# Kernel optimization log

Hardware: AMD Instinct MI355X
Metric: run time of the kernel (lower is better)

Reference implementation:

```python
import jax, jax.numpy as jnp
import numpy as np

H = 4096   # hidden_size
V = 4      # vocab_size (Dyck-2)
OUT = 4    # output_size
MS = 104   # memory_size (stack depth)
MD = 3     # memory_dim (stack element width)


def setup_inputs() -> dict:
    key = jax.random.key(0)
    ks = jax.random.split(key, 17)
    s = 1.0 / np.sqrt(H)
    f32 = jnp.float32
    return {
        "inp": jax.random.randint(ks[0], (1,), 0, H),
        "hidden0": jax.random.normal(ks[1], (1, 1, H), f32),
        "stack": jax.random.normal(ks[2], (MS, MD), f32),
        "emb": (jax.random.normal(ks[3], (H, V), f32) * s),      # nn.Embedding(H, V)
        "w_ih": (jax.random.normal(ks[4], (3 * H, V), f32) * s),  # GRU input weights
        "w_hh": (jax.random.normal(ks[5], (3 * H, H), f32) * s),  # GRU hidden weights
        "b_ih": (jax.random.normal(ks[6], (3 * H,), f32) * s),
        "b_hh": (jax.random.normal(ks[7], (3 * H,), f32) * s),
        "w_y": (jax.random.normal(ks[8], (OUT, H), f32) * s),
        "b_y": (jax.random.normal(ks[9], (OUT,), f32) * s),
        "w_n": (jax.random.normal(ks[10], (MD, H), f32) * s),
        "b_n": (jax.random.normal(ks[11], (MD,), f32) * s),
        "w_a": (jax.random.normal(ks[12], (2, H), f32) * s),
        "b_a": (jax.random.normal(ks[13], (2,), f32) * s),
        "w_sh": (jax.random.normal(ks[14], (H, MD), f32) * s),
        "b_sh": (jax.random.normal(ks[15], (H,), f32) * s),
    }


def reference(inp, hidden0, stack, emb, w_ih, w_hh, b_ih, b_hh,
              w_y, b_y, w_n, b_n, w_a, b_a, w_sh, b_sh):
    # embedded = embedding(inp).view(1,1,-1) -> work with flat (V,)
    x = emb[inp[0]]                                   # (V,)
    # hidden_bar = W_sh(stack[0]) + hidden0
    h_bar = (w_sh @ stack[0] + b_sh) + hidden0[0, 0]  # (H,)
    # one GRU step (PyTorch gate order: r, z, n)
    gi = w_ih @ x + b_ih                              # (3H,)
    gh = w_hh @ h_bar + b_hh                          # (3H,)
    i_r, i_z, i_n = jnp.split(gi, 3)
    h_r, h_z, h_n = jnp.split(gh, 3)
    r = jax.nn.sigmoid(i_r + h_r)
    z = jax.nn.sigmoid(i_z + h_z)
    n = jnp.tanh(i_n + r * h_n)
    h = (1.0 - z) * n + z * h_bar                     # (H,) = ht = hidden
    # heads
    output = jax.nn.sigmoid(w_y @ h + b_y).reshape(1, OUT)
    action = jax.nn.softmax(w_a @ h + b_a)            # (2,) push/pop weights
    new_elt = jax.nn.sigmoid(w_n @ h + b_n).reshape(1, MD)
    # differentiable stack update
    push_side = jnp.concatenate([new_elt, stack[:-1]], axis=0)          # (MS, MD)
    pop_side = jnp.concatenate([stack[1:], jnp.zeros((1, MD), stack.dtype)], axis=0)
    new_stack = action[0] * push_side + action[1] * pop_side
    hidden = h.reshape(1, 1, H)
    return output, hidden, new_stack
```

## Files before the change

kernel.cpp:

```cpp
#include <hip/hip_runtime.h>
#include <hip/hip_bf16.h>

#define H  4096
#define V  4
#define OUT_N 4
#define MS 104
#define MD 3

__device__ __forceinline__ float b2f(unsigned short u) {
    return __uint_as_float(((unsigned int)u) << 16);
}
__device__ __forceinline__ float ldf(const void* p, size_t i, bool is_f32) {
    return is_f32 ? ((const float*)p)[i] : b2f(((const unsigned short*)p)[i]);
}
__device__ __forceinline__ void stf(void* p, size_t i, bool is_f32, float v) {
    if (is_f32) ((float*)p)[i] = v;
    else        ((__hip_bfloat16*)p)[i] = __float2bfloat16(v);
}

__device__ __forceinline__ bool detect_f32(const void* w_hh) {
    const unsigned short* w = (const unsigned short*)w_hh;
    const int lane = threadIdx.x & 63;
    int bad = 0;
    #pragma unroll
    for (int i = 0; i < 16; ++i) {
        const float v = b2f(w[lane + (i << 6)]);
        if (!(fabsf(v) < 1.0e6f)) bad = 1;
    }
    return __ballot(bad) != 0ull;
}

__device__ __forceinline__ float dot8(uint4 a, float4 h0, float4 h1) {
    return __uint_as_float(a.x << 16)          * h0.x
         + __uint_as_float(a.x & 0xffff0000u)  * h0.y
         + __uint_as_float(a.y << 16)          * h0.z
         + __uint_as_float(a.y & 0xffff0000u)  * h0.w
         + __uint_as_float(a.z << 16)          * h1.x
         + __uint_as_float(a.z & 0xffff0000u)  * h1.y
         + __uint_as_float(a.w << 16)          * h1.z
         + __uint_as_float(a.w & 0xffff0000u)  * h1.w;
}

__global__ __launch_bounds__(256) void hbar_kernel(
    const void* __restrict__ w_sh, const void* __restrict__ b_sh,
    const void* __restrict__ hidden0, const void* __restrict__ stack,
    const void* __restrict__ w_hh, float* __restrict__ h_bar) {
    const bool f32 = detect_f32(w_hh);
    const float s0 = ldf(stack, 0, f32);
    const float s1 = ldf(stack, 1, f32);
    const float s2 = ldf(stack, 2, f32);
    const int j = blockIdx.x * 256 + threadIdx.x;
    h_bar[j] = ldf(w_sh, (size_t)j * 3 + 0, f32) * s0
             + ldf(w_sh, (size_t)j * 3 + 1, f32) * s1
             + ldf(w_sh, (size_t)j * 3 + 2, f32) * s2
             + ldf(b_sh, j, f32) + ldf(hidden0, j, f32);
}

__global__ __launch_bounds__(256) void gru_kernel(
    const int*  __restrict__ inp,  const void* __restrict__ emb,
    const void* __restrict__ w_ih, const void* __restrict__ w_hh,
    const void* __restrict__ b_ih, const void* __restrict__ b_hh,
    const float* __restrict__ h_bar, float* __restrict__ h_f32,
    void* __restrict__ out) {
    const bool f32 = detect_f32(w_hh);
    const int wave = threadIdx.x >> 6, lane = threadIdx.x & 63;
    const int k = (blockIdx.x << 2) + wave;

    float ar = 0.f, az = 0.f, an = 0.f;
    if (f32) {
        const float4* W  = (const float4*)w_hh;
        const float4* HB = (const float4*)h_bar;
        const size_t q0 = (size_t)k           * (H / 4);
        const size_t q1 = (size_t)(k + H)     * (H / 4);
        const size_t q2 = (size_t)(k + 2 * H) * (H / 4);
        #pragma unroll 4
        for (int it = 0; it < H / 256; ++it) {
            const int i = (it << 6) + lane;
            const float4 hb = HB[i];
            const float4 a = W[q0 + i];
            const float4 b = W[q1 + i];
            const float4 c = W[q2 + i];
            ar += a.x * hb.x + a.y * hb.y + a.z * hb.z + a.w * hb.w;
            az += b.x * hb.x + b.y * hb.y + b.z * hb.z + b.w * hb.w;
            an += c.x * hb.x + c.y * hb.y + c.z * hb.z + c.w * hb.w;
        }
    } else {
        const uint4*  W  = (const uint4*)w_hh;
        const float4* HB = (const float4*)h_bar;
        const size_t q0 = (size_t)k           * (H / 8);
        const size_t q1 = (size_t)(k + H)     * (H / 8);
        const size_t q2 = (size_t)(k + 2 * H) * (H / 8);
        #pragma unroll 2
        for (int it = 0; it < H / 512; ++it) {
            const int i = (it << 6) + lane;
            const float4 h0 = HB[2 * i], h1 = HB[2 * i + 1];
            ar += dot8(W[q0 + i], h0, h1);
            az += dot8(W[q1 + i], h0, h1);
            an += dot8(W[q2 + i], h0, h1);
        }
    }

    #pragma unroll
    for (int off = 32; off > 0; off >>= 1) {
        ar += __shfl_down(ar, off);
        az += __shfl_down(az, off);
        an += __shfl_down(an, off);
    }

    if (lane == 0) {
        const int idx = inp[0];
        float x[V];
        #pragma unroll
        for (int c = 0; c < V; ++c) x[c] = ldf(emb, (size_t)idx * V + c, f32);

        float gi[3];
        #pragma unroll
        for (int g = 0; g < 3; ++g) {
            float acc = ldf(b_ih, (size_t)(k + g * H), f32);
            #pragma unroll
            for (int c = 0; c < V; ++c)
                acc += ldf(w_ih, (size_t)(k + g * H) * V + c, f32) * x[c];
            gi[g] = acc;
        }
        const float ghr = ar + ldf(b_hh, (size_t)k,           f32);
        const float ghz = az + ldf(b_hh, (size_t)(k + H),     f32);
        const float ghn = an + ldf(b_hh, (size_t)(k + 2 * H), f32);

        const float r = 1.f / (1.f + expf(-(gi[0] + ghr)));
        const float z = 1.f / (1.f + expf(-(gi[1] + ghz)));
        const float n = tanhf(gi[2] + r * ghn);
        const float hk = (1.f - z) * n + z * h_bar[k];

        h_f32[k] = hk;
        stf(out, (size_t)(OUT_N + k), f32, hk);
    }
}

__global__ __launch_bounds__(1024) void heads_kernel(
    const float* __restrict__ h,
    const void* __restrict__ w_y, const void* __restrict__ b_y,
    const void* __restrict__ w_a, const void* __restrict__ b_a,
    const void* __restrict__ w_n, const void* __restrict__ b_n,
    const void* __restrict__ stack, const void* __restrict__ w_hh,
    void* __restrict__ out) {
    const bool f32 = detect_f32(w_hh);
    const int t = threadIdx.x, wave = t >> 6, lane = t & 63;

    __shared__ float scal[9];
    if (wave < 9) {
        const void* base; size_t row;
        if (wave < 4)      { base = w_y; row = (size_t)wave * H; }
        else if (wave < 6) { base = w_a; row = (size_t)(wave - 4) * H; }
        else               { base = w_n; row = (size_t)(wave - 6) * H; }

        float acc = 0.f;
        if (f32) {
            const float4* W  = (const float4*)((const float*)base + row);
            const float4* Hv = (const float4*)h;
            #pragma unroll 4
            for (int it = 0; it < H / 256; ++it) {
                const int i = (it << 6) + lane;
                const float4 a = W[i], hb = Hv[i];
                acc += a.x * hb.x + a.y * hb.y + a.z * hb.z + a.w * hb.w;
            }
        } else {
            const uint4*  W  = (const uint4*)((const unsigned short*)base + row);
            const float4* Hv = (const float4*)h;
            #pragma unroll 2
            for (int it = 0; it < H / 512; ++it) {
                const int i = (it << 6) + lane;
                acc += dot8(W[i], Hv[2 * i], Hv[2 * i + 1]);
            }
        }
        #pragma unroll
        for (int off = 32; off > 0; off >>= 1) acc += __shfl_down(acc, off);
        if (lane == 0) scal[wave] = acc;
    }
    __syncthreads();

    __shared__ float act0, act1, ne[MD];
    if (t == 0) {
        const float a0 = scal[4] + ldf(b_a, 0, f32);
        const float a1 = scal[5] + ldf(b_a, 1, f32);
        const float m  = fmaxf(a0, a1);
        const float e0 = expf(a0 - m), e1 = expf(a1 - m);
        const float inv = 1.f / (e0 + e1);
        act0 = e0 * inv; act1 = e1 * inv;
    }
    if (t < OUT_N)
        stf(out, (size_t)t, f32,
            1.f / (1.f + expf(-(scal[t] + ldf(b_y, t, f32)))));
    if (t < MD)
        ne[t] = 1.f / (1.f + expf(-(scal[6 + t] + ldf(b_n, t, f32))));
    __syncthreads();

    const float a0 = act0, a1 = act1;
    for (int idx = t; idx < MS * MD; idx += 1024) {
        const int i = idx / MD;
        const int d = idx - i * MD;
        const float push = (i == 0)      ? ne[d] : ldf(stack, (size_t)(idx - MD), f32);
        const float pop  = (i == MS - 1) ? 0.f   : ldf(stack, (size_t)(idx + MD), f32);
        stf(out, (size_t)(OUT_N + H + idx), f32, a0 * push + a1 * pop);
    }
}

extern "C" void kernel_launch(void* const* d_in, const int* in_sizes, int n_in,
                              void* d_out, int out_size, void* d_ws, size_t ws_size,
                              hipStream_t stream) {
    const int* inp      = (const int*)d_in[0];
    const void* hidden0 = d_in[1];
    const void* stack   = d_in[2];
    const void* emb     = d_in[3];
    const void* w_ih    = d_in[4];
    const void* w_hh    = d_in[5];
    const void* b_ih    = d_in[6];
    const void* b_hh    = d_in[7];
    const void* w_y     = d_in[8];
    const void* b_y     = d_in[9];
    const void* w_n     = d_in[10];
    const void* b_n     = d_in[11];
    const void* w_a     = d_in[12];
    const void* b_a     = d_in[13];
    const void* w_sh    = d_in[14];
    const void* b_sh    = d_in[15];

    float* h_bar = (float*)d_ws;
    float* h     = h_bar + H;

    hbar_kernel<<<H / 256, 256, 0, stream>>>(w_sh, b_sh, hidden0, stack,
                                             w_hh, h_bar);
    gru_kernel<<<H / 4, 256, 0, stream>>>(inp, emb, w_ih, w_hh, b_ih, b_hh,
                                          h_bar, h, d_out);
    heads_kernel<<<1, 1024, 0, stream>>>(h, w_y, b_y, w_a, b_a, w_n, b_n,
                                         stack, w_hh, d_out);
}
```

Baseline: 314.1 us.

## Fuse h_bar computation into GRU kernel with LDS-staged hidden vector

Merges the separate h_bar kernel into the GRU matvec kernel. Each block now recomputes the full h_bar vector into shared memory, then assigns one wave per gate row (2 hidden units × 3 gates per block) and reduces through LDS. This removes one launch and the global round trip for h_bar. In exchange, every one of the 2048 blocks redundantly reads w_sh, b_sh and hidden0 before it can start streaming w_hh. The 16KB of LDS per block may also limit occupancy.

```diff
diff --git a/kernel.cpp b/kernel.cpp
--- a/kernel.cpp
+++ b/kernel.cpp
@@ -6,6 +6,9 @@
 #define OUT_N 4
 #define MS 104
 #define MD 3
+
+#define KPB 2
+#define TPB (KPB * 3 * 64)
 
 __device__ __forceinline__ float b2f(unsigned short u) {
     return __uint_as_float(((unsigned int)u) << 16);
@@ -41,73 +44,64 @@
          + __uint_as_float(a.w & 0xffff0000u)  * h1.w;
 }
 
-__global__ __launch_bounds__(256) void hbar_kernel(
+__global__ __launch_bounds__(TPB) void gru_fused_kernel(
+    const int*  __restrict__ inp,  const void* __restrict__ emb,
+    const void* __restrict__ w_ih, const void* __restrict__ w_hh,
+    const void* __restrict__ b_ih, const void* __restrict__ b_hh,
     const void* __restrict__ w_sh, const void* __restrict__ b_sh,
     const void* __restrict__ hidden0, const void* __restrict__ stack,
-    const void* __restrict__ w_hh, float* __restrict__ h_bar) {
+    float* __restrict__ h_f32, void* __restrict__ out) {
     const bool f32 = detect_f32(w_hh);
+    const int t = threadIdx.x;
+    const int wave = t >> 6, lane = t & 63;
+    const int k0 = blockIdx.x * KPB;
+
+    __shared__ float hb_lds[H];
+    __shared__ float red[KPB][3];
+
     const float s0 = ldf(stack, 0, f32);
     const float s1 = ldf(stack, 1, f32);
     const float s2 = ldf(stack, 2, f32);
-    const int j = blockIdx.x * 256 + threadIdx.x;
-    h_bar[j] = ldf(w_sh, (size_t)j * 3 + 0, f32) * s0
-             + ldf(w_sh, (size_t)j * 3 + 1, f32) * s1
-             + ldf(w_sh, (size_t)j * 3 + 2, f32) * s2
-             + ldf(b_sh, j, f32) + ldf(hidden0, j, f32);
-}
-
-__global__ __launch_bounds__(256) void gru_kernel(
-    const int*  __restrict__ inp,  const void* __restrict__ emb,
-    const void* __restrict__ w_ih, const void* __restrict__ w_hh,
-    const void* __restrict__ b_ih, const void* __restrict__ b_hh,
-    const float* __restrict__ h_bar, float* __restrict__ h_f32,
-    void* __restrict__ out) {
-    const bool f32 = detect_f32(w_hh);
-    const int wave = threadIdx.x >> 6, lane = threadIdx.x & 63;
-    const int k = (blockIdx.x << 2) + wave;
-
-    float ar = 0.f, az = 0.f, an = 0.f;
+    for (int j = t; j < H; j += TPB) {
+        hb_lds[j] = ldf(w_sh, (size_t)j * 3 + 0, f32) * s0
+                  + ldf(w_sh, (size_t)j * 3 + 1, f32) * s1
+                  + ldf(w_sh, (size_t)j * 3 + 2, f32) * s2
+                  + ldf(b_sh, j, f32) + ldf(hidden0, j, f32);
+    }
+    __syncthreads();
+
+    const int g  = wave % 3;
+    const int kk = wave / 3;
+    const int row = g * H + k0 + kk;
+
+    float acc = 0.f;
     if (f32) {
-        const float4* W  = (const float4*)w_hh;
-        const float4* HB = (const float4*)h_bar;
-        const size_t q0 = (size_t)k           * (H / 4);
-        const size_t q1 = (size_t)(k + H)     * (H / 4);
-        const size_t q2 = (size_t)(k + 2 * H) * (H / 4);
+        const float4* W  = (const float4*)w_hh + (size_t)row * (H / 4);
+        const float4* HB = (const float4*)hb_lds;
         #pragma unroll 4
         for (int it = 0; it < H / 256; ++it) {
             const int i = (it << 6) + lane;
-            const float4 hb = HB[i];
-            const float4 a = W[q0 + i];
-            const float4 b = W[q1 + i];
-            const float4 c = W[q2 + i];
-            ar += a.x * hb.x + a.y * hb.y + a.z * hb.z + a.w * hb.w;
-            az += b.x * hb.x + b.y * hb.y + b.z * hb.z + b.w * hb.w;
-            an += c.x * hb.x + c.y * hb.y + c.z * hb.z + c.w * hb.w;
+            const float4 a = W[i], hb = HB[i];
+            acc += a.x * hb.x + a.y * hb.y + a.z * hb.z + a.w * hb.w;
         }
     } else {
-        const uint4*  W  = (const uint4*)w_hh;
-        const float4* HB = (const float4*)h_bar;
-        const size_t q0 = (size_t)k           * (H / 8);
-        const size_t q1 = (size_t)(k + H)     * (H / 8);
-        const size_t q2 = (size_t)(k + 2 * H) * (H / 8);
-        #pragma unroll 2
+        const uint4*  W  = (const uint4*)w_hh + (size_t)row * (H / 8);
+        const float4* HB = (const float4*)hb_lds;
+        #pragma unroll 4
         for (int it = 0; it < H / 512; ++it) {
             const int i = (it << 6) + lane;
-            const float4 h0 = HB[2 * i], h1 = HB[2 * i + 1];
-            ar += dot8(W[q0 + i], h0, h1);
-            az += dot8(W[q1 + i], h0, h1);
-            an += dot8(W[q2 + i], h0, h1);
-        }
-    }
-
+            acc += dot8(W[i], HB[2 * i], HB[2 * i + 1]);
+        }
+    }
     #pragma unroll
-    for (int off = 32; off > 0; off >>= 1) {
-        ar += __shfl_down(ar, off);
-        az += __shfl_down(az, off);
-        an += __shfl_down(an, off);
-    }
-
-    if (lane == 0) {
+    for (int off = 32; off > 0; off >>= 1) acc += __shfl_down(acc, off);
+    if (lane == 0) red[kk][g] = acc;
+    __syncthreads();
+
+    if (t < KPB) {
+        const int k = k0 + t;
+        const float sr = red[t][0], sz = red[t][1], sn = red[t][2];
+
         const int idx = inp[0];
         float x[V];
         #pragma unroll
@@ -115,21 +109,21 @@
 
         float gi[3];
         #pragma unroll
-        for (int g = 0; g < 3; ++g) {
-            float acc = ldf(b_ih, (size_t)(k + g * H), f32);
+        for (int gg = 0; gg < 3; ++gg) {
+            float a = ldf(b_ih, (size_t)(k + gg * H), f32);
             #pragma unroll
             for (int c = 0; c < V; ++c)
-                acc += ldf(w_ih, (size_t)(k + g * H) * V + c, f32) * x[c];
-            gi[g] = acc;
-        }
-        const float ghr = ar + ldf(b_hh, (size_t)k,           f32);
-        const float ghz = az + ldf(b_hh, (size_t)(k + H),     f32);
-        const float ghn = an + ldf(b_hh, (size_t)(k + 2 * H), f32);
+                a += ldf(w_ih, (size_t)(k + gg * H) * V + c, f32) * x[c];
+            gi[gg] = a;
+        }
+        const float ghr = sr + ldf(b_hh, (size_t)k,           f32);
+        const float ghz = sz + ldf(b_hh, (size_t)(k + H),     f32);
+        const float ghn = sn + ldf(b_hh, (size_t)(k + 2 * H), f32);
 
         const float r = 1.f / (1.f + expf(-(gi[0] + ghr)));
         const float z = 1.f / (1.f + expf(-(gi[1] + ghz)));
         const float n = tanhf(gi[2] + r * ghn);
-        const float hk = (1.f - z) * n + z * h_bar[k];
+        const float hk = (1.f - z) * n + z * hb_lds[k];
 
         h_f32[k] = hk;
         stf(out, (size_t)(OUT_N + k), f32, hk);
@@ -224,13 +218,10 @@
     const void* w_sh    = d_in[14];
     const void* b_sh    = d_in[15];
 
-    float* h_bar = (float*)d_ws;
-    float* h     = h_bar + H;
-
-    hbar_kernel<<<H / 256, 256, 0, stream>>>(w_sh, b_sh, hidden0, stack,
-                                             w_hh, h_bar);
-    gru_kernel<<<H / 4, 256, 0, stream>>>(inp, emb, w_ih, w_hh, b_ih, b_hh,
-                                          h_bar, h, d_out);
+    float* h = (float*)d_ws;
+
+    gru_fused_kernel<<<H / KPB, TPB, 0, stream>>>(
+        inp, emb, w_ih, w_hh, b_ih, b_hh, w_sh, b_sh, hidden0, stack, h, d_out);
     heads_kernel<<<1, 1024, 0, stream>>>(h, w_y, b_y, w_a, b_a, w_n, b_n,
                                          stack, w_hh, d_out);
 }
```

Result: slower. 321.4 us (+2.3%).
